# Performance work log

Hardware: AMD Instinct MI355X
Metric: run time of the kernel (lower is better)

Reference implementation:

```python
import jax, jax.numpy as jnp
import numpy as np

ABILITY_SCALE = 3.0

def setup_inputs() -> dict:
    key = jax.random.key(0)
    ks = jax.random.split(key, 20)
    Q, K, M, KD, VD, FD, B, S = 5000, 4, 64, 128, 256, 128, 128, 1024
    g = lambda k, shape: jax.random.normal(k, shape, jnp.float32) * 0.05
    return dict(
        q_data=jax.random.randint(ks[0], (B, S), 0, Q + 1),
        r_data=jax.random.randint(ks[1], (B, S), 0, K),
        q_embed_table=g(ks[2], (Q + 1, KD)),
        key_memory=g(ks[3], (M, KD)),
        init_value_memory=g(ks[4], (M, VD)),
        W_value=g(ks[5], (2 * Q, VD)), b_value=jnp.zeros((VD,), jnp.float32),
        W_erase=g(ks[6], (VD, VD)), b_erase=jnp.zeros((VD,), jnp.float32),
        W_add=g(ks[7], (VD, VD)), b_add=jnp.zeros((VD,), jnp.float32),
        W_summary=g(ks[8], (VD + KD, FD)), b_summary=jnp.zeros((FD,), jnp.float32),
        W_theta=g(ks[9], (FD, 1)), b_theta=jnp.zeros((1,), jnp.float32),
        W_beta=g(ks[10], (KD, K - 1)), b_beta=jnp.zeros((K - 1,), jnp.float32),
        W_disc=g(ks[11], (FD + KD, 1)), b_disc=jnp.zeros((1,), jnp.float32),
        W_c1=g(ks[12], (K + 1, 64)), b_c1=jnp.zeros((64,), jnp.float32),  # irt_dim = 1+1+(K-1)
        W_c2=g(ks[13], (64, 32)), b_c2=jnp.zeros((32,), jnp.float32),
        coral_w=g(ks[14], (32, 1)), coral_b=jnp.zeros((K - 1,), jnp.float32),
    )


def reference(q_data, r_data, q_embed_table, key_memory, init_value_memory,
              W_value, b_value, W_erase, b_erase, W_add, b_add,
              W_summary, b_summary, W_theta, b_theta, W_beta, b_beta,
              W_disc, b_disc, W_c1, b_c1, W_c2, b_c2, coral_w, coral_b):
    B, S = q_data.shape
    Q = W_value.shape[0] // 2
    K = coral_b.shape[0] + 1
    Mv0 = jnp.broadcast_to(init_value_memory[None], (B,) + init_value_memory.shape)

    def step(Mv, qr):
        q_t, r_t = qr  # (B,), (B,)
        qe = q_embed_table[q_t]                                   # (B, KD)
        q1h = jax.nn.one_hot(q_t, Q + 1, dtype=jnp.float32)[:, 1:]  # (B, Q), drop padding id 0
        scale = (r_t.astype(jnp.float32) / (K - 1))[:, None]
        x = jnp.concatenate([q1h, q1h * scale], axis=-1)          # ordered embedding (B, 2Q)
        ve = x @ W_value + b_value                                # (B, VD)
        w = jax.nn.softmax(qe @ key_memory.T, axis=-1)            # (B, M) correlation weight
        read = jnp.einsum('bm,bmv->bv', w, Mv)                    # memory read
        summary = jnp.tanh(jnp.concatenate([read, qe], -1) @ W_summary + b_summary)
        theta = (summary @ W_theta + b_theta)[:, 0] * ABILITY_SCALE
        betas = qe @ W_beta + b_beta                              # (B, K-1)
        alpha = jax.nn.softplus((jnp.concatenate([summary, qe], -1) @ W_disc + b_disc)[:, 0])
        # CORAL head on IRT params
        feat = jnp.concatenate([theta[:, None], alpha[:, None], betas], -1)  # (B, K+1)
        h = jax.nn.relu(feat @ W_c1 + b_c1)
        h = jax.nn.relu(h @ W_c2 + b_c2)
        logits = h @ coral_w + coral_b                            # (B, K-1), shared weight + thresholds
        cum = jnp.cumprod(jax.nn.sigmoid(logits), axis=-1)        # CORN: P(y > k)
        probs = jnp.concatenate([1.0 - cum[:, :1], cum[:, :-1] - cum[:, 1:], cum[:, -1:]], -1)
        # memory write (erase/add)
        erase = jax.nn.sigmoid(ve @ W_erase + b_erase)
        add = jnp.tanh(ve @ W_add + b_add)
        Mv = Mv * (1.0 - w[:, :, None] * erase[:, None, :]) + w[:, :, None] * add[:, None, :]
        return Mv, (theta, betas, alpha, probs, logits)

    _, (thetas, betas, alphas, probs, logits) = jax.lax.scan(
        step, Mv0, (q_data.T, r_data.T))
    tr = lambda a: jnp.swapaxes(a, 0, 1)  # (S, B, ...) -> (B, S, ...)
    return (tr(thetas), tr(betas), tr(alphas), tr(probs), tr(logits))
```

## Files before the change

kernel.cpp:

```cpp
#include <hip/hip_runtime.h>
#include <math.h>

#define BB 128
#define SS 1024
#define MM 64
#define KDIM 128
#define VDIM 256
#define FDIM 128
#define QNUM 5000
#define QD 5001
#define RROWS (4 * QD)

#define QB 16
#define NEA ((QD + QB - 1) / QB)
#define NPRE (NEA + QD + 128)

#define TW 16
#define NWIN (SS / TW)

typedef _Float16 half2_t __attribute__((ext_vector_type(2)));
typedef float f2 __attribute__((ext_vector_type(2)));
typedef _Float16 f16x8 __attribute__((ext_vector_type(8)));
typedef float f32x4 __attribute__((ext_vector_type(4)));

#if defined(__has_builtin)
#if __has_builtin(__builtin_elementwise_fma)
#define HAVE_EFMA 1
#endif
#endif

__device__ __forceinline__ f2 pkfma(f2 a, f2 b, f2 c) {
#ifdef HAVE_EFMA
  return __builtin_elementwise_fma(a, b, c);
#else
  f2 r; r.x = fmaf(a.x, b.x, c.x); r.y = fmaf(a.y, b.y, c.y); return r;
#endif
}

__device__ __forceinline__ float sigmoidf_(float x) { return 1.0f / (1.0f + expf(-x)); }
__device__ __forceinline__ float softplusf_(float x) { return (x > 20.0f) ? x : log1pf(expf(x)); }

__global__ __launch_bounds__(256) void k_pre(
    const float* __restrict__ Wv, const float* __restrict__ bv,
    const float* __restrict__ We, const float* __restrict__ be,
    const float* __restrict__ Wa, const float* __restrict__ ba,
    const float* __restrict__ q_embed, const float* __restrict__ key_mem,
    const float* __restrict__ W_summary, const float* __restrict__ b_summary,
    const float* __restrict__ W_disc,
    const float* __restrict__ W_beta, const float* __restrict__ b_beta,
    float2* __restrict__ EA, float* __restrict__ w_tab,
    float* __restrict__ Sq_tab, float* __restrict__ aq_tab,
    float* __restrict__ beta_tab, _Float16* __restrict__ Wh)
{
  const int tid = threadIdx.x;
  const int blk = blockIdx.x;
  __shared__ __align__(16) float smem[2 * QB * 256];
  __shared__ float s_small[KDIM + MM + FDIM];

  if (blk < NEA) {
    float* su = smem;
    float* sd = smem + QB * 256;
    const int qbase = blk * QB;
#pragma unroll
    for (int j = 0; j < QB; ++j) {
      const int q = qbase + j;
      float u = bv[tid], d = 0.f;
      if (q >= 1 && q < QD) {
        u += Wv[(size_t)(q - 1) * VDIM + tid];
        d = Wv[(size_t)(QNUM + q - 1) * VDIM + tid] * (1.0f / 3.0f);
      }
      su[j * 256 + tid] = u;
      sd[j * 256 + tid] = d;
    }
    __syncthreads();
    f2 aB[QB], aD[QB];
#pragma unroll
    for (int j = 0; j < QB; ++j) { aB[j] = (f2){0.f, 0.f}; aD[j] = (f2){0.f, 0.f}; }
    for (int i = 0; i < 256; i += 4) {
      f2 w0, w1, w2, w3;
      w0.x = We[(i + 0) * VDIM + tid]; w0.y = Wa[(i + 0) * VDIM + tid];
      w1.x = We[(i + 1) * VDIM + tid]; w1.y = Wa[(i + 1) * VDIM + tid];
      w2.x = We[(i + 2) * VDIM + tid]; w2.y = Wa[(i + 2) * VDIM + tid];
      w3.x = We[(i + 3) * VDIM + tid]; w3.y = Wa[(i + 3) * VDIM + tid];
#pragma unroll
      for (int j = 0; j < QB; ++j) {
        const float4 uu = *(const float4*)&su[j * 256 + i];
        const float4 dd = *(const float4*)&sd[j * 256 + i];
        aB[j] = pkfma((f2){uu.x, uu.x}, w0, aB[j]);
        aD[j] = pkfma((f2){dd.x, dd.x}, w0, aD[j]);
        aB[j] = pkfma((f2){uu.y, uu.y}, w1, aB[j]);
        aD[j] = pkfma((f2){dd.y, dd.y}, w1, aD[j]);
        aB[j] = pkfma((f2){uu.z, uu.z}, w2, aB[j]);
        aD[j] = pkfma((f2){dd.z, dd.z}, w2, aD[j]);
        aB[j] = pkfma((f2){uu.w, uu.w}, w3, aB[j]);
        aD[j] = pkfma((f2){dd.w, dd.w}, w3, aD[j]);
      }
    }
    const float bev = be[tid], bav = ba[tid];
#pragma unroll
    for (int j = 0; j < QB; ++j) {
      const int q = qbase + j;
      if (q < QD) {
        const float pe0 = aB[j].x + bev, pa0 = aB[j].y + bav;
        const float de = aD[j].x, da = aD[j].y;
#pragma unroll
        for (int r = 0; r < 4; ++r) {
          float2 p;
          p.x = sigmoidf_(fmaf((float)r, de, pe0));
          p.y = tanhf(fmaf((float)r, da, pa0));
          EA[(size_t)(r * QD + q) * VDIM + tid] = p;
        }
      }
    }
  } else if (blk < NEA + QD) {
    const int q = blk - NEA;
    const int wave = tid >> 6, l = tid & 63;
    float* s_key  = smem;
    float* qe     = s_small;
    float* slog   = s_small + KDIM;
    float* s_half = s_small + KDIM + MM;
    for (int i = tid; i < MM * KDIM; i += 256) s_key[i] = key_mem[i];
    if (tid < KDIM) qe[tid] = q_embed[(size_t)q * KDIM + tid];
    __syncthreads();
    {
      const int m = tid >> 2, j = tid & 3;
      const float* krow = s_key + m * KDIM + j * 32;
      const float* qrow = qe + j * 32;
      float acc = 0.f;
#pragma unroll
      for (int k = 0; k < 32; ++k) {
        const int i = (k + tid) & 31;
        acc = fmaf(qrow[i], krow[i], acc);
      }
      acc += __shfl_xor(acc, 1);
      acc += __shfl_xor(acc, 2);
      if (j == 0) slog[m] = acc;
    }
    __syncthreads();
    if (wave == 0) {
      const float x = slog[l];
      float mx = x;
#pragma unroll
      for (int o = 32; o; o >>= 1) mx = fmaxf(mx, __shfl_xor(mx, o));
      const float e = expf(x - mx);
      float s = e;
#pragma unroll
      for (int o = 32; o; o >>= 1) s += __shfl_xor(s, o);
      w_tab[(size_t)q * MM + l] = e / s;
    } else if (wave == 1) {
      float p = qe[l] * W_disc[KDIM + l] + qe[64 + l] * W_disc[KDIM + 64 + l];
#pragma unroll
      for (int o = 32; o; o >>= 1) p += __shfl_xor(p, o);
      if (l == 0) aq_tab[q] = p;
    } else if (wave == 2) {
      float p0 = qe[l] * W_beta[l * 3 + 0] + qe[64 + l] * W_beta[(64 + l) * 3 + 0];
      float p1 = qe[l] * W_beta[l * 3 + 1] + qe[64 + l] * W_beta[(64 + l) * 3 + 1];
      float p2 = qe[l] * W_beta[l * 3 + 2] + qe[64 + l] * W_beta[(64 + l) * 3 + 2];
#pragma unroll
      for (int o = 32; o; o >>= 1) {
        p0 += __shfl_xor(p0, o); p1 += __shfl_xor(p1, o); p2 += __shfl_xor(p2, o);
      }
      if (l == 0) {
        beta_tab[(size_t)q * 3 + 0] = p0 + b_beta[0];
        beta_tab[(size_t)q * 3 + 1] = p1 + b_beta[1];
        beta_tab[(size_t)q * 3 + 2] = p2 + b_beta[2];
      }
    }
    {
      const int f = tid & 127, h = tid >> 7;
      float acc = 0.f;
#pragma unroll 8
      for (int k = 0; k < 64; ++k)
        acc = fmaf(qe[h * 64 + k], W_summary[(size_t)(VDIM + h * 64 + k) * FDIM + f], acc);
      if (h == 1) s_half[f] = acc;
      __syncthreads();
      if (h == 0) Sq_tab[(size_t)q * FDIM + f] = acc + s_half[f] + b_summary[f];
    }
  } else {
    const int e = (blk - NEA - QD) * 256 + tid;
    const int f = e >> 8, k = e & 255;
    Wh[(size_t)f * 256 + k] = (_Float16)W_summary[(size_t)k * FDIM + f];
  }
}

typedef union { f32x4 v4; f2 h[2]; } Wp;

__global__ __launch_bounds__(512, 4) void k_rec10(
    const int* __restrict__ q_data, const int* __restrict__ r_data,
    const float* __restrict__ init_mv,
    const float2* __restrict__ EA, const float* __restrict__ w_tab,
    _Float16* __restrict__ Rd)
{
  const int tid = threadIdx.x;
  const int lane = tid & 63;
  const int wv = tid >> 6;
  const int b = blockIdx.x >> 2, vc = blockIdx.x & 3;
  const int vv = vc * 64 + lane;
  const int m0 = wv * 8;

  __shared__ int s_off[SS + 32];
  __shared__ int s_q64[SS + 32];
  __shared__ __align__(16) float s_w[2][TW][64];
  __shared__ __align__(16) float s_red[TW][8][64];

  for (int i = tid; i < SS; i += 512) {
    const int q = q_data[b * SS + i];
    const int r = r_data[b * SS + i];
    s_off[i] = (r * QD + q) * (int)(VDIM * sizeof(float2));
    s_q64[i] = q << 6;
  }
  if (tid < 32) { s_off[SS + tid] = 0; s_q64[SS + tid] = 0; }
  __syncthreads();

  {
    const float wa = w_tab[s_q64[wv] + lane];
    const float wb = w_tab[s_q64[wv + 8] + lane];
    s_w[0][wv][lane] = wa;
    s_w[0][wv + 8][lane] = wb;
  }

  f2 mv2[4];
#pragma unroll
  for (int k = 0; k < 4; ++k) {
    mv2[k].x = init_mv[(size_t)(m0 + 2 * k) * VDIM + vv];
    mv2[k].y = init_mv[(size_t)(m0 + 2 * k + 1) * VDIM + vv];
  }

  const char* EAv = (const char*)EA + (size_t)vv * sizeof(float2);

  __syncthreads();

  f2 ear[8];
#pragma unroll
  for (int j = 0; j < 8; ++j)
    ear[j] = *(const f2*)(EAv + (size_t)(unsigned)s_off[j]);

  Wp wl[2], wh[2];

  for (int win = 0; win < NWIN; ++win) {
    const int buf = win & 1;
    const int t0 = win * TW;
    const int tn = ((win + 1) & (NWIN - 1)) * TW + wv;
    const float wstA = w_tab[s_q64[tn] + lane];
    const float wstB = w_tab[s_q64[tn + 8] + lane];
    wl[0].v4 = *(const f32x4*)&s_w[buf][0][m0];
    wh[0].v4 = *(const f32x4*)&s_w[buf][0][m0 + 4];
    wl[1].v4 = *(const f32x4*)&s_w[buf][1][m0];
    wh[1].v4 = *(const f32x4*)&s_w[buf][1][m0 + 4];
#pragma unroll
    for (int tt = 0; tt < TW; ++tt) {
      const int t = t0 + tt;
      const f2 ea = ear[tt & 7];
      const Wp wlo = wl[tt & 1], whi = wh[tt & 1];
      if (tt < TW - 2) {
        wl[tt & 1].v4 = *(const f32x4*)&s_w[buf][tt + 2][m0];
        wh[tt & 1].v4 = *(const f32x4*)&s_w[buf][tt + 2][m0 + 4];
      }
      ear[tt & 7] = *(const f2*)(EAv + (size_t)(unsigned)s_off[t + 8]);
      const f2 e2 = {ea.x, ea.x}, a2 = {ea.y, ea.y};
      f2 rdA = wlo.h[0] * mv2[0];
      rdA = pkfma(wlo.h[1], mv2[1], rdA);
      f2 rdB = whi.h[0] * mv2[2];
      rdB = pkfma(whi.h[1], mv2[3], rdB);
      mv2[0] = pkfma(wlo.h[0], pkfma(-e2, mv2[0], a2), mv2[0]);
      mv2[1] = pkfma(wlo.h[1], pkfma(-e2, mv2[1], a2), mv2[1]);
      mv2[2] = pkfma(whi.h[0], pkfma(-e2, mv2[2], a2), mv2[2]);
      mv2[3] = pkfma(whi.h[1], pkfma(-e2, mv2[3], a2), mv2[3]);
      const f2 rs = rdA + rdB;
      s_red[tt][wv][lane] = rs.x + rs.y;
    }
    __syncthreads();
    {
      s_w[buf ^ 1][wv][lane] = wstA;
      s_w[buf ^ 1][wv + 8][lane] = wstB;
      const int rt = tid >> 5;
      const int vp = (tid & 31) * 2;
      f2 s = *(const f2*)&s_red[rt][0][vp];
#pragma unroll
      for (int k = 1; k < 8; ++k) s += *(const f2*)&s_red[rt][k][vp];
      half2_t hv; hv[0] = (_Float16)s.x; hv[1] = (_Float16)s.y;
      *(half2_t*)&Rd[((size_t)b * SS + t0 + rt) * VDIM + vc * 64 + vp] = hv;
    }
    __syncthreads();
  }
}

__global__ __launch_bounds__(256) void k_head(
    const int* __restrict__ q_data,
    const _Float16* __restrict__ Rd, const _Float16* __restrict__ Wh,
    const float* __restrict__ Sq_tab, const float* __restrict__ aq_tab,
    const float* __restrict__ beta_tab,
    const float* __restrict__ W_theta, const float* __restrict__ b_theta,
    const float* __restrict__ W_disc, const float* __restrict__ b_disc,
    const float* __restrict__ W_c1, const float* __restrict__ b_c1,
    const float* __restrict__ W_c2, const float* __restrict__ b_c2,
    const float* __restrict__ coral_w, const float* __restrict__ coral_b,
    float* __restrict__ out)
{
  const int tid = threadIdx.x;
  const int w = tid >> 6, l = tid & 63;
  const int rowbase = blockIdx.x * 64;
  const int b = rowbase >> 10;
  const int t0 = rowbase & (SS - 1);

  __shared__ __align__(16) _Float16 s_A[64 * 256];
  __shared__ __align__(16) _Float16 s_sum[64 * 128];
  __shared__ __align__(16) float s_h1[4][64];
  __shared__ int   s_q[64];
  __shared__ float s_aq[64];
  __shared__ float s_be[64][3];

  {
    const uint4* src = (const uint4*)(Rd + (size_t)rowbase * VDIM);
    uint4* dst = (uint4*)s_A;
    for (int i = tid; i < (64 * 256 * 2) / 16; i += 256) dst[i] = src[i];
  }
  if (tid < 64) {
    const int q = q_data[b * SS + t0 + tid];
    s_q[tid] = q;
    s_aq[tid] = aq_tab[q];
    s_be[tid][0] = beta_tab[(size_t)q * 3 + 0];
    s_be[tid][1] = beta_tab[(size_t)q * 3 + 1];
    s_be[tid][2] = beta_tab[(size_t)q * 3 + 2];
  }
  __syncthreads();

  {
    const int quad = l >> 4, r16 = l & 15;
    const int mrow = w * 16 + r16;
    f32x4 acc[8];
#pragma unroll
    for (int nt = 0; nt < 8; ++nt) acc[nt] = (f32x4){0.f, 0.f, 0.f, 0.f};
#pragma unroll
    for (int ks = 0; ks < 8; ++ks) {
      const f16x8 afrag = *(const f16x8*)(s_A + mrow * 256 + ks * 32 + quad * 8);
#pragma unroll
      for (int nt = 0; nt < 8; ++nt) {
        const int n = nt * 16 + r16;
        const f16x8 bfrag = *(const f16x8*)(Wh + (size_t)n * 256 + ks * 32 + quad * 8);
        acc[nt] = __builtin_amdgcn_mfma_f32_16x16x32_f16(afrag, bfrag, acc[nt], 0, 0, 0);
      }
    }
#pragma unroll
    for (int nt = 0; nt < 8; ++nt) {
#pragma unroll
      for (int reg = 0; reg < 4; ++reg) {
        const int row = w * 16 + quad * 4 + reg;
        const int col = nt * 16 + r16;
        const float val = acc[nt][reg] + Sq_tab[(size_t)s_q[row] * FDIM + col];
        s_sum[row * 128 + col] = (_Float16)tanhf(val);
      }
    }
  }
  __syncthreads();

  const float tw0 = W_theta[l], tw1 = W_theta[64 + l], tb = b_theta[0];
  const float dw0 = W_disc[l], dw1 = W_disc[64 + l], db = b_disc[0];
  float wc1reg[5];
#pragma unroll
  for (int i = 0; i < 5; ++i) wc1reg[i] = W_c1[i * 64 + l];
  const float bc1 = b_c1[l];
  const int jj = l >> 1, hh2 = l & 1;
  float wc2reg[32];
#pragma unroll
  for (int i = 0; i < 32; ++i) wc2reg[i] = W_c2[(hh2 * 32 + i) * 32 + jj];
  const float bc2 = b_c2[jj];
  const float cw = coral_w[jj];
  const float cb0 = coral_b[0], cb1 = coral_b[1], cb2 = coral_b[2];

  float* out_theta = out;
  float* out_beta  = out + (size_t)BB * SS;
  float* out_alpha = out + (size_t)BB * SS * 4;
  float* out_probs = out + (size_t)BB * SS * 5;
  float* out_logit = out + (size_t)BB * SS * 9;

  for (int rr = 0; rr < 16; ++rr) {
    const int r = w * 16 + rr;
    const float su0 = (float)s_sum[r * 128 + l];
    const float su1 = (float)s_sum[r * 128 + 64 + l];
    float at = su0 * tw0 + su1 * tw1;
    float ad = su0 * dw0 + su1 * dw1;
#pragma unroll
    for (int o = 32; o; o >>= 1) { at += __shfl_xor(at, o); ad += __shfl_xor(ad, o); }
    const float theta = (at + tb) * 3.0f;
    const float alpha = softplusf_(ad + s_aq[r] + db);
    const float be0 = s_be[r][0], be1 = s_be[r][1], be2 = s_be[r][2];
    float h1 = bc1;
    h1 = fmaf(theta, wc1reg[0], h1);
    h1 = fmaf(alpha, wc1reg[1], h1);
    h1 = fmaf(be0, wc1reg[2], h1);
    h1 = fmaf(be1, wc1reg[3], h1);
    h1 = fmaf(be2, wc1reg[4], h1);
    h1 = fmaxf(h1, 0.f);
    s_h1[w][l] = h1;
    float hacc = hh2 ? 0.f : bc2;
    const float4* h4 = (const float4*)s_h1[w];
#pragma unroll
    for (int k = 0; k < 8; ++k) {
      const float4 hv = h4[(hh2 << 3) + k];
      hacc = fmaf(hv.x, wc2reg[4 * k + 0], hacc);
      hacc = fmaf(hv.y, wc2reg[4 * k + 1], hacc);
      hacc = fmaf(hv.z, wc2reg[4 * k + 2], hacc);
      hacc = fmaf(hv.w, wc2reg[4 * k + 3], hacc);
    }
    hacc += __shfl_xor(hacc, 1);
    const float h2 = fmaxf(hacc, 0.f);
    float p = h2 * cw * 0.5f;
#pragma unroll
    for (int o = 32; o; o >>= 1) p += __shfl_xor(p, o);
    if (l == 0) {
      const float z = p;
      const float l0 = z + cb0, l1 = z + cb1, l2 = z + cb2;
      const float s0 = sigmoidf_(l0), s1 = sigmoidf_(l1), s2 = sigmoidf_(l2);
      const float q0 = s0, q1 = s0 * s1, q2 = s0 * s1 * s2;
      const size_t bt = (size_t)rowbase + r;
      out_theta[bt] = theta;
      out_alpha[bt] = alpha;
      out_beta[bt * 3 + 0] = be0;
      out_beta[bt * 3 + 1] = be1;
      out_beta[bt * 3 + 2] = be2;
      out_logit[bt * 3 + 0] = l0;
      out_logit[bt * 3 + 1] = l1;
      out_logit[bt * 3 + 2] = l2;
      out_probs[bt * 4 + 0] = 1.f - q0;
      out_probs[bt * 4 + 1] = q0 - q1;
      out_probs[bt * 4 + 2] = q1 - q2;
      out_probs[bt * 4 + 3] = q2;
    }
  }
}

extern "C" void kernel_launch(void* const* d_in, const int* in_sizes, int n_in,
                              void* d_out, int out_size, void* d_ws, size_t ws_size,
                              hipStream_t stream) {
  const int*   q_data    = (const int*)d_in[0];
  const int*   r_data    = (const int*)d_in[1];
  const float* q_embed   = (const float*)d_in[2];
  const float* key_mem   = (const float*)d_in[3];
  const float* init_mv   = (const float*)d_in[4];
  const float* W_value   = (const float*)d_in[5];
  const float* b_value   = (const float*)d_in[6];
  const float* W_erase   = (const float*)d_in[7];
  const float* b_erase   = (const float*)d_in[8];
  const float* W_add     = (const float*)d_in[9];
  const float* b_add     = (const float*)d_in[10];
  const float* W_summary = (const float*)d_in[11];
  const float* b_summary = (const float*)d_in[12];
  const float* W_theta   = (const float*)d_in[13];
  const float* b_theta   = (const float*)d_in[14];
  const float* W_beta    = (const float*)d_in[15];
  const float* b_beta    = (const float*)d_in[16];
  const float* W_disc    = (const float*)d_in[17];
  const float* b_disc    = (const float*)d_in[18];
  const float* W_c1      = (const float*)d_in[19];
  const float* b_c1      = (const float*)d_in[20];
  const float* W_c2      = (const float*)d_in[21];
  const float* b_c2      = (const float*)d_in[22];
  const float* coral_w   = (const float*)d_in[23];
  const float* coral_b   = (const float*)d_in[24];

  float* ws = (float*)d_ws;
  size_t off = 0;
  float2* EA      = (float2*)(ws + off); off += (size_t)RROWS * VDIM * 2;
  float* w_tab    = ws + off; off += (size_t)QD * MM;
  float* Sq_tab   = ws + off; off += (size_t)QD * FDIM;
  float* aq_tab   = ws + off; off += 5120;
  float* beta_tab = ws + off; off += 15104;
  _Float16* Wh = (_Float16*)(ws + off); off += (VDIM * FDIM) / 2;
  _Float16* Rd = (_Float16*)(ws + off);

  k_pre<<<dim3(NPRE), dim3(256), 0, stream>>>(
      W_value, b_value, W_erase, b_erase, W_add, b_add,
      q_embed, key_mem, W_summary, b_summary, W_disc, W_beta, b_beta,
      EA, w_tab, Sq_tab, aq_tab, beta_tab, Wh);

  k_rec10<<<dim3(BB * 4), dim3(512), 0, stream>>>(
      q_data, r_data, init_mv, EA, w_tab, Rd);

  k_head<<<dim3((BB * SS) / 64), dim3(256), 0, stream>>>(
      q_data, Rd, Wh, Sq_tab, aq_tab, beta_tab,
      W_theta, b_theta, W_disc, b_disc,
      W_c1, b_c1, W_c2, b_c2, coral_w, coral_b, (float*)d_out);
}
```

Measured before the change: 544.6 us.

## Store attention weights in fp16 and vectorize offset prefetch in recurrence

Softmax read weights are stored as fp16 in the precomputed table and in shared memory, so each step loads a single 16-byte vector of eight weights instead of two float4 loads, and the per-window global gather of weights moves half the bytes. The EA gather offsets are now read four at a time as an int4 from shared memory rather than one scalar per step, with the sentinel padding widened to match. This trims LDS traffic and instruction count in the serial inner loop, at the cost of fp16 rounding of the attention weights and extra conversion instructions per step.

```diff
diff --git a/kernel.cpp b/kernel.cpp
--- a/kernel.cpp
+++ b/kernel.cpp
@@ -48,7 +48,7 @@
     const float* __restrict__ W_summary, const float* __restrict__ b_summary,
     const float* __restrict__ W_disc,
     const float* __restrict__ W_beta, const float* __restrict__ b_beta,
-    float2* __restrict__ EA, float* __restrict__ w_tab,
+    float2* __restrict__ EA, _Float16* __restrict__ w_tab,
     float* __restrict__ Sq_tab, float* __restrict__ aq_tab,
     float* __restrict__ beta_tab, _Float16* __restrict__ Wh)
 {
@@ -146,7 +146,7 @@
       float s = e;
 #pragma unroll
       for (int o = 32; o; o >>= 1) s += __shfl_xor(s, o);
-      w_tab[(size_t)q * MM + l] = e / s;
+      w_tab[(size_t)q * MM + l] = (_Float16)(e / s);
     } else if (wave == 1) {
       float p = qe[l] * W_disc[KDIM + l] + qe[64 + l] * W_disc[KDIM + 64 + l];
 #pragma unroll
@@ -183,12 +183,10 @@
   }
 }
 
-typedef union { f32x4 v4; f2 h[2]; } Wp;
-
-__global__ __launch_bounds__(512, 4) void k_rec10(
+__global__ __launch_bounds__(512, 4) void k_rec13(
     const int* __restrict__ q_data, const int* __restrict__ r_data,
     const float* __restrict__ init_mv,
-    const float2* __restrict__ EA, const float* __restrict__ w_tab,
+    const float2* __restrict__ EA, const _Float16* __restrict__ w_tab,
     _Float16* __restrict__ Rd)
 {
   const int tid = threadIdx.x;
@@ -198,9 +196,9 @@
   const int vv = vc * 64 + lane;
   const int m0 = wv * 8;
 
-  __shared__ int s_off[SS + 32];
-  __shared__ int s_q64[SS + 32];
-  __shared__ __align__(16) float s_w[2][TW][64];
+  __shared__ int s_off[SS + 64];
+  __shared__ int s_q64[SS + 64];
+  __shared__ __align__(16) _Float16 s_w16[2][TW][64];
   __shared__ __align__(16) float s_red[TW][8][64];
 
   for (int i = tid; i < SS; i += 512) {
@@ -209,14 +207,14 @@
     s_off[i] = (r * QD + q) * (int)(VDIM * sizeof(float2));
     s_q64[i] = q << 6;
   }
-  if (tid < 32) { s_off[SS + tid] = 0; s_q64[SS + tid] = 0; }
+  if (tid < 64) { s_off[SS + tid] = 0; s_q64[SS + tid] = 0; }
   __syncthreads();
 
   {
-    const float wa = w_tab[s_q64[wv] + lane];
-    const float wb = w_tab[s_q64[wv + 8] + lane];
-    s_w[0][wv][lane] = wa;
-    s_w[0][wv + 8][lane] = wb;
+    const _Float16 wa = w_tab[s_q64[wv] + lane];
+    const _Float16 wb = w_tab[s_q64[wv + 8] + lane];
+    s_w16[0][wv][lane] = wa;
+    s_w16[0][wv + 8][lane] = wb;
   }
 
   f2 mv2[4];
@@ -235,44 +233,48 @@
   for (int j = 0; j < 8; ++j)
     ear[j] = *(const f2*)(EAv + (size_t)(unsigned)s_off[j]);
 
-  Wp wl[2], wh[2];
+  f16x8 wr[2];
 
   for (int win = 0; win < NWIN; ++win) {
     const int buf = win & 1;
     const int t0 = win * TW;
     const int tn = ((win + 1) & (NWIN - 1)) * TW + wv;
-    const float wstA = w_tab[s_q64[tn] + lane];
-    const float wstB = w_tab[s_q64[tn + 8] + lane];
-    wl[0].v4 = *(const f32x4*)&s_w[buf][0][m0];
-    wh[0].v4 = *(const f32x4*)&s_w[buf][0][m0 + 4];
-    wl[1].v4 = *(const f32x4*)&s_w[buf][1][m0];
-    wh[1].v4 = *(const f32x4*)&s_w[buf][1][m0 + 4];
+    const _Float16 wstA = w_tab[s_q64[tn] + lane];
+    const _Float16 wstB = w_tab[s_q64[tn + 8] + lane];
+    wr[0] = *(const f16x8*)&s_w16[buf][0][m0];
+    wr[1] = *(const f16x8*)&s_w16[buf][1][m0];
+    int4 pf;
 #pragma unroll
     for (int tt = 0; tt < TW; ++tt) {
-      const int t = t0 + tt;
+      if ((tt & 3) == 0) pf = *(const int4*)&s_off[t0 + tt + 8];
       const f2 ea = ear[tt & 7];
-      const Wp wlo = wl[tt & 1], whi = wh[tt & 1];
-      if (tt < TW - 2) {
-        wl[tt & 1].v4 = *(const f32x4*)&s_w[buf][tt + 2][m0];
-        wh[tt & 1].v4 = *(const f32x4*)&s_w[buf][tt + 2][m0 + 4];
-      }
-      ear[tt & 7] = *(const f2*)(EAv + (size_t)(unsigned)s_off[t + 8]);
+      const f16x8 wf = wr[tt & 1];
+      if (tt < TW - 2)
+        wr[tt & 1] = *(const f16x8*)&s_w16[buf][tt + 2][m0];
+      {
+        const int po = (tt & 3) == 0 ? pf.x : (tt & 3) == 1 ? pf.y : (tt & 3) == 2 ? pf.z : pf.w;
+        ear[tt & 7] = *(const f2*)(EAv + (size_t)(unsigned)po);
+      }
+      const f2 w0 = {(float)wf[0], (float)wf[1]};
+      const f2 w1 = {(float)wf[2], (float)wf[3]};
+      const f2 w2 = {(float)wf[4], (float)wf[5]};
+      const f2 w3 = {(float)wf[6], (float)wf[7]};
       const f2 e2 = {ea.x, ea.x}, a2 = {ea.y, ea.y};
-      f2 rdA = wlo.h[0] * mv2[0];
-      rdA = pkfma(wlo.h[1], mv2[1], rdA);
-      f2 rdB = whi.h[0] * mv2[2];
-      rdB = pkfma(whi.h[1], mv2[3], rdB);
-      mv2[0] = pkfma(wlo.h[0], pkfma(-e2, mv2[0], a2), mv2[0]);
-      mv2[1] = pkfma(wlo.h[1], pkfma(-e2, mv2[1], a2), mv2[1]);
-      mv2[2] = pkfma(whi.h[0], pkfma(-e2, mv2[2], a2), mv2[2]);
-      mv2[3] = pkfma(whi.h[1], pkfma(-e2, mv2[3], a2), mv2[3]);
+      f2 rdA = w0 * mv2[0];
+      rdA = pkfma(w1, mv2[1], rdA);
+      f2 rdB = w2 * mv2[2];
+      rdB = pkfma(w3, mv2[3], rdB);
+      mv2[0] = pkfma(w0, pkfma(-e2, mv2[0], a2), mv2[0]);
+      mv2[1] = pkfma(w1, pkfma(-e2, mv2[1], a2), mv2[1]);
+      mv2[2] = pkfma(w2, pkfma(-e2, mv2[2], a2), mv2[2]);
+      mv2[3] = pkfma(w3, pkfma(-e2, mv2[3], a2), mv2[3]);
       const f2 rs = rdA + rdB;
       s_red[tt][wv][lane] = rs.x + rs.y;
     }
     __syncthreads();
     {
-      s_w[buf ^ 1][wv][lane] = wstA;
-      s_w[buf ^ 1][wv + 8][lane] = wstB;
+      s_w16[buf ^ 1][wv][lane] = wstA;
+      s_w16[buf ^ 1][wv + 8][lane] = wstB;
       const int rt = tid >> 5;
       const int vp = (tid & 31) * 2;
       f2 s = *(const f2*)&s_red[rt][0][vp];
@@ -462,7 +464,7 @@
   float* ws = (float*)d_ws;
   size_t off = 0;
   float2* EA      = (float2*)(ws + off); off += (size_t)RROWS * VDIM * 2;
-  float* w_tab    = ws + off; off += (size_t)QD * MM;
+  _Float16* w_tab = (_Float16*)(ws + off); off += (size_t)QD * MM;
   float* Sq_tab   = ws + off; off += (size_t)QD * FDIM;
   float* aq_tab   = ws + off; off += 5120;
   float* beta_tab = ws + off; off += 15104;
@@ -474,7 +476,7 @@
       q_embed, key_mem, W_summary, b_summary, W_disc, W_beta, b_beta,
       EA, w_tab, Sq_tab, aq_tab, beta_tab, Wh);
 
-  k_rec10<<<dim3(BB * 4), dim3(512), 0, stream>>>(
+  k_rec13<<<dim3(BB * 4), dim3(512), 0, stream>>>(
       q_data, r_data, init_mv, EA, w_tab, Rd);
 
   k_head<<<dim3((BB * SS) / 64), dim3(256), 0, stream>>>(
```

After: 548.4 us. No clear change (+0.7%).

## Halve recurrence blocks, each thread handling two value columns

Applied to the files above, without the earlier changes.

The recurrence kernel now uses two blocks per batch element instead of four, and each thread updates two value columns (v and v+64) packed into float2. The per-step weight, read-offset and shared-memory reduction costs are spread over twice as much work. Offsets are also fetched four at a time from shared memory. The trade-off is fewer blocks (256 instead of 512), which may leave CUs idle, plus more registers per thread. Launch bounds drop to 2 blocks per CU to match.

```diff
diff --git a/kernel.cpp b/kernel.cpp
--- a/kernel.cpp
+++ b/kernel.cpp
@@ -185,7 +185,7 @@
 
 typedef union { f32x4 v4; f2 h[2]; } Wp;
 
-__global__ __launch_bounds__(512, 4) void k_rec10(
+__global__ __launch_bounds__(512, 2) void k_rec14(
     const int* __restrict__ q_data, const int* __restrict__ r_data,
     const float* __restrict__ init_mv,
     const float2* __restrict__ EA, const float* __restrict__ w_tab,
@@ -194,14 +194,14 @@
   const int tid = threadIdx.x;
   const int lane = tid & 63;
   const int wv = tid >> 6;
-  const int b = blockIdx.x >> 2, vc = blockIdx.x & 3;
-  const int vv = vc * 64 + lane;
+  const int b = blockIdx.x >> 1, vc = blockIdx.x & 1;
+  const int vv = vc * 128 + lane;
   const int m0 = wv * 8;
 
   __shared__ int s_off[SS + 32];
   __shared__ int s_q64[SS + 32];
   __shared__ __align__(16) float s_w[2][TW][64];
-  __shared__ __align__(16) float s_red[TW][8][64];
+  __shared__ __align__(16) f2 s_red[TW][8][64];
 
   for (int i = tid; i < SS; i += 512) {
     const int q = q_data[b * SS + i];
@@ -219,21 +219,23 @@
     s_w[0][wv + 8][lane] = wb;
   }
 
-  f2 mv2[4];
-#pragma unroll
-  for (int k = 0; k < 4; ++k) {
-    mv2[k].x = init_mv[(size_t)(m0 + 2 * k) * VDIM + vv];
-    mv2[k].y = init_mv[(size_t)(m0 + 2 * k + 1) * VDIM + vv];
+  f2 mv[8];
+#pragma unroll
+  for (int k = 0; k < 8; ++k) {
+    mv[k].x = init_mv[(size_t)(m0 + k) * VDIM + vv];
+    mv[k].y = init_mv[(size_t)(m0 + k) * VDIM + vv + 64];
   }
 
   const char* EAv = (const char*)EA + (size_t)vv * sizeof(float2);
 
   __syncthreads();
 
-  f2 ear[8];
-#pragma unroll
-  for (int j = 0; j < 8; ++j)
-    ear[j] = *(const f2*)(EAv + (size_t)(unsigned)s_off[j]);
+  f2 eaL[8], eaH[8];
+#pragma unroll
+  for (int j = 0; j < 8; ++j) {
+    eaL[j] = *(const f2*)(EAv + (size_t)(unsigned)s_off[j]);
+    eaH[j] = *(const f2*)(EAv + (size_t)(unsigned)s_off[j] + 64 * sizeof(float2));
+  }
 
   Wp wl[2], wh[2];
 
@@ -247,39 +249,58 @@
     wh[0].v4 = *(const f32x4*)&s_w[buf][0][m0 + 4];
     wl[1].v4 = *(const f32x4*)&s_w[buf][1][m0];
     wh[1].v4 = *(const f32x4*)&s_w[buf][1][m0 + 4];
+    int4 pf;
 #pragma unroll
     for (int tt = 0; tt < TW; ++tt) {
-      const int t = t0 + tt;
-      const f2 ea = ear[tt & 7];
+      if ((tt & 3) == 0) pf = *(const int4*)&s_off[t0 + tt + 8];
+      const f2 lo = eaL[tt & 7], hi = eaH[tt & 7];
       const Wp wlo = wl[tt & 1], whi = wh[tt & 1];
       if (tt < TW - 2) {
         wl[tt & 1].v4 = *(const f32x4*)&s_w[buf][tt + 2][m0];
         wh[tt & 1].v4 = *(const f32x4*)&s_w[buf][tt + 2][m0 + 4];
       }
-      ear[tt & 7] = *(const f2*)(EAv + (size_t)(unsigned)s_off[t + 8]);
-      const f2 e2 = {ea.x, ea.x}, a2 = {ea.y, ea.y};
-      f2 rdA = wlo.h[0] * mv2[0];
-      rdA = pkfma(wlo.h[1], mv2[1], rdA);
-      f2 rdB = whi.h[0] * mv2[2];
-      rdB = pkfma(whi.h[1], mv2[3], rdB);
-      mv2[0] = pkfma(wlo.h[0], pkfma(-e2, mv2[0], a2), mv2[0]);
-      mv2[1] = pkfma(wlo.h[1], pkfma(-e2, mv2[1], a2), mv2[1]);
-      mv2[2] = pkfma(whi.h[0], pkfma(-e2, mv2[2], a2), mv2[2]);
-      mv2[3] = pkfma(whi.h[1], pkfma(-e2, mv2[3], a2), mv2[3]);
-      const f2 rs = rdA + rdB;
-      s_red[tt][wv][lane] = rs.x + rs.y;
+      {
+        const int po = (tt & 3) == 0 ? pf.x : (tt & 3) == 1 ? pf.y : (tt & 3) == 2 ? pf.z : pf.w;
+        eaL[tt & 7] = *(const f2*)(EAv + (size_t)(unsigned)po);
+        eaH[tt & 7] = *(const f2*)(EAv + (size_t)(unsigned)po + 64 * sizeof(float2));
+      }
+      const f2 e2 = {lo.x, hi.x}, a2 = {lo.y, hi.y};
+      const f2 w0 = {wlo.v4[0], wlo.v4[0]}, w1 = {wlo.v4[1], wlo.v4[1]};
+      const f2 w2 = {wlo.v4[2], wlo.v4[2]}, w3 = {wlo.v4[3], wlo.v4[3]};
+      const f2 w4 = {whi.v4[0], whi.v4[0]}, w5 = {whi.v4[1], whi.v4[1]};
+      const f2 w6 = {whi.v4[2], whi.v4[2]}, w7 = {whi.v4[3], whi.v4[3]};
+      f2 rdA = w0 * mv[0];
+      rdA = pkfma(w1, mv[1], rdA);
+      rdA = pkfma(w2, mv[2], rdA);
+      rdA = pkfma(w3, mv[3], rdA);
+      f2 rdB = w4 * mv[4];
+      rdB = pkfma(w5, mv[5], rdB);
+      rdB = pkfma(w6, mv[6], rdB);
+      rdB = pkfma(w7, mv[7], rdB);
+      mv[0] = pkfma(w0, pkfma(-e2, mv[0], a2), mv[0]);
+      mv[1] = pkfma(w1, pkfma(-e2, mv[1], a2), mv[1]);
+      mv[2] = pkfma(w2, pkfma(-e2, mv[2], a2), mv[2]);
+      mv[3] = pkfma(w3, pkfma(-e2, mv[3], a2), mv[3]);
+      mv[4] = pkfma(w4, pkfma(-e2, mv[4], a2), mv[4]);
+      mv[5] = pkfma(w5, pkfma(-e2, mv[5], a2), mv[5]);
+      mv[6] = pkfma(w6, pkfma(-e2, mv[6], a2), mv[6]);
+      mv[7] = pkfma(w7, pkfma(-e2, mv[7], a2), mv[7]);
+      s_red[tt][wv][lane] = rdA + rdB;
     }
     __syncthreads();
     {
       s_w[buf ^ 1][wv][lane] = wstA;
       s_w[buf ^ 1][wv + 8][lane] = wstB;
       const int rt = tid >> 5;
-      const int vp = (tid & 31) * 2;
-      f2 s = *(const f2*)&s_red[rt][0][vp];
-#pragma unroll
-      for (int k = 1; k < 8; ++k) s += *(const f2*)&s_red[rt][k][vp];
-      half2_t hv; hv[0] = (_Float16)s.x; hv[1] = (_Float16)s.y;
-      *(half2_t*)&Rd[((size_t)b * SS + t0 + rt) * VDIM + vc * 64 + vp] = hv;
+      const int sl0 = (tid & 31) * 2;
+      f32x4 s = *(const f32x4*)&s_red[rt][0][sl0];
+#pragma unroll
+      for (int k = 1; k < 8; ++k) s += *(const f32x4*)&s_red[rt][k][sl0];
+      half2_t hA; hA[0] = (_Float16)s[0]; hA[1] = (_Float16)s[2];
+      half2_t hB; hB[0] = (_Float16)s[1]; hB[1] = (_Float16)s[3];
+      _Float16* rrow = Rd + ((size_t)b * SS + t0 + rt) * VDIM + vc * 128;
+      *(half2_t*)(rrow + sl0) = hA;
+      *(half2_t*)(rrow + 64 + sl0) = hB;
     }
     __syncthreads();
   }
@@ -474,7 +495,7 @@
       q_embed, key_mem, W_summary, b_summary, W_disc, W_beta, b_beta,
       EA, w_tab, Sq_tab, aq_tab, beta_tab, Wh);
 
-  k_rec10<<<dim3(BB * 4), dim3(512), 0, stream>>>(
+  k_rec14<<<dim3(BB * 2), dim3(512), 0, stream>>>(
       q_data, r_data, init_mv, EA, w_tab, Rd);
 
   k_head<<<dim3((BB * SS) / 64), dim3(256), 0, stream>>>(
```

Result: no change. 548.8 us (+0.8%).

## Split recurrence over memory-slot halves with partial read outputs summed in head

Applied to the files above, without the earlier changes.

Adds a new recurrence kernel that gives each block half of the 64 memory slots and 128 value columns, not all 64 slots and 64 columns. Each half writes its partial read vector to a separate fp16 buffer, and the head kernel adds the two buffers while loading them into shared memory. Each lane now covers two value columns, so one gathered erase/add pointer serves twice the work, and the per-step reduction is stored as fp16 in shared memory. The cost is a second global read buffer, extra fp16 rounding before the final sum, and lower occupancy (launch bounds 2 instead of 4). The path is chosen at runtime only when the workspace is large enough, otherwise the old kernel runs.

```diff
diff --git a/kernel.cpp b/kernel.cpp
--- a/kernel.cpp
+++ b/kernel.cpp
@@ -184,6 +184,116 @@
 }
 
 typedef union { f32x4 v4; f2 h[2]; } Wp;
+typedef union { uint2 u; half2_t h[2]; } H4;
+
+__global__ __launch_bounds__(512, 2) void k_rec15(
+    const int* __restrict__ q_data, const int* __restrict__ r_data,
+    const float* __restrict__ init_mv,
+    const float2* __restrict__ EA, const float* __restrict__ w_tab,
+    _Float16* __restrict__ Rd0, _Float16* __restrict__ Rd1)
+{
+  const int tid = threadIdx.x;
+  const int lane = tid & 63;
+  const int wv = tid >> 6;
+  const int idx = blockIdx.x;
+  const int b = idx >> 2, vc = (idx >> 1) & 1, mh = idx & 1;
+  const int vv = vc * 128 + lane;
+  const int mql = mh * 32;
+  const int m0 = mql + wv * 4;
+  _Float16* __restrict__ Rdh = mh ? Rd1 : Rd0;
+
+  __shared__ int s_off[SS + 32];
+  __shared__ int s_q64[SS + 32];
+  __shared__ __align__(16) float s_w[2][TW][32];
+  __shared__ __align__(16) half2_t s_red16[TW][8][64];
+
+  for (int i = tid; i < SS; i += 512) {
+    const int q = q_data[b * SS + i];
+    const int r = r_data[b * SS + i];
+    s_off[i] = (r * QD + q) * (int)(VDIM * sizeof(float2));
+    s_q64[i] = q << 6;
+  }
+  if (tid < 32) { s_off[SS + tid] = 0; s_q64[SS + tid] = 0; }
+  __syncthreads();
+
+  const int srow = tid >> 5, scol = tid & 31;
+  s_w[0][srow][scol] = w_tab[s_q64[srow] + mql + scol];
+
+  f2 mv[4];
+#pragma unroll
+  for (int k = 0; k < 4; ++k) {
+    mv[k].x = init_mv[(size_t)(m0 + k) * VDIM + vv];
+    mv[k].y = init_mv[(size_t)(m0 + k) * VDIM + vv + 64];
+  }
+
+  const char* EAv = (const char*)EA + (size_t)vv * sizeof(float2);
+
+  __syncthreads();
+
+  f2 eaL[8], eaH[8];
+#pragma unroll
+  for (int j = 0; j < 8; ++j) {
+    eaL[j] = *(const f2*)(EAv + (size_t)(unsigned)s_off[j]);
+    eaH[j] = *(const f2*)(EAv + (size_t)(unsigned)s_off[j] + 64 * sizeof(float2));
+  }
+
+  f32x4 wr[2];
+
+  for (int win = 0; win < NWIN; ++win) {
+    const int buf = win & 1;
+    const int t0 = win * TW;
+    const int wn = ((win + 1) & (NWIN - 1)) * TW;
+    const float wst = w_tab[s_q64[wn + srow] + mql + scol];
+    wr[0] = *(const f32x4*)&s_w[buf][0][wv * 4];
+    wr[1] = *(const f32x4*)&s_w[buf][1][wv * 4];
+    int4 pf;
+#pragma unroll
+    for (int tt = 0; tt < TW; ++tt) {
+      if ((tt & 3) == 0) pf = *(const int4*)&s_off[t0 + tt + 8];
+      const f2 lo = eaL[tt & 7], hi = eaH[tt & 7];
+      const f32x4 wq = wr[tt & 1];
+      if (tt < TW - 2)
+        wr[tt & 1] = *(const f32x4*)&s_w[buf][tt + 2][wv * 4];
+      {
+        const int po = (tt & 3) == 0 ? pf.x : (tt & 3) == 1 ? pf.y : (tt & 3) == 2 ? pf.z : pf.w;
+        eaL[tt & 7] = *(const f2*)(EAv + (size_t)(unsigned)po);
+        eaH[tt & 7] = *(const f2*)(EAv + (size_t)(unsigned)po + 64 * sizeof(float2));
+      }
+      const f2 e2 = {lo.x, hi.x}, a2 = {lo.y, hi.y};
+      const f2 w0 = {wq[0], wq[0]}, w1 = {wq[1], wq[1]};
+      const f2 w2 = {wq[2], wq[2]}, w3 = {wq[3], wq[3]};
+      f2 rd = w0 * mv[0];
+      rd = pkfma(w1, mv[1], rd);
+      rd = pkfma(w2, mv[2], rd);
+      rd = pkfma(w3, mv[3], rd);
+      mv[0] = pkfma(w0, pkfma(-e2, mv[0], a2), mv[0]);
+      mv[1] = pkfma(w1, pkfma(-e2, mv[1], a2), mv[1]);
+      mv[2] = pkfma(w2, pkfma(-e2, mv[2], a2), mv[2]);
+      mv[3] = pkfma(w3, pkfma(-e2, mv[3], a2), mv[3]);
+      half2_t h; h[0] = (_Float16)rd.x; h[1] = (_Float16)rd.y;
+      s_red16[tt][wv][lane] = h;
+    }
+    __syncthreads();
+    {
+      s_w[buf ^ 1][srow][scol] = wst;
+      const int rt = tid >> 5;
+      const int sl0 = (tid & 31) * 2;
+      float a0 = 0.f, a1 = 0.f, b0 = 0.f, b1 = 0.f;
+#pragma unroll
+      for (int k = 0; k < 8; ++k) {
+        H4 u; u.u = *(const uint2*)&s_red16[rt][k][sl0];
+        a0 += (float)u.h[0][0]; a1 += (float)u.h[0][1];
+        b0 += (float)u.h[1][0]; b1 += (float)u.h[1][1];
+      }
+      half2_t hA; hA[0] = (_Float16)a0; hA[1] = (_Float16)b0;
+      half2_t hB; hB[0] = (_Float16)a1; hB[1] = (_Float16)b1;
+      _Float16* rrow = Rdh + ((size_t)b * SS + t0 + rt) * VDIM + vc * 128;
+      *(half2_t*)(rrow + sl0) = hA;
+      *(half2_t*)(rrow + 64 + sl0) = hB;
+    }
+    __syncthreads();
+  }
+}
 
 __global__ __launch_bounds__(512, 4) void k_rec10(
     const int* __restrict__ q_data, const int* __restrict__ r_data,
@@ -287,7 +397,8 @@
 
 __global__ __launch_bounds__(256) void k_head(
     const int* __restrict__ q_data,
-    const _Float16* __restrict__ Rd, const _Float16* __restrict__ Wh,
+    const _Float16* __restrict__ Rd0, const _Float16* __restrict__ Rd1, const int two,
+    const _Float16* __restrict__ Wh,
     const float* __restrict__ Sq_tab, const float* __restrict__ aq_tab,
     const float* __restrict__ beta_tab,
     const float* __restrict__ W_theta, const float* __restrict__ b_theta,
@@ -311,9 +422,19 @@
   __shared__ float s_be[64][3];
 
   {
-    const uint4* src = (const uint4*)(Rd + (size_t)rowbase * VDIM);
+    typedef union { uint4 u; f16x8 h; } U8;
+    const uint4* src0 = (const uint4*)(Rd0 + (size_t)rowbase * VDIM);
+    const uint4* src1 = (const uint4*)(Rd1 + (size_t)rowbase * VDIM);
     uint4* dst = (uint4*)s_A;
-    for (int i = tid; i < (64 * 256 * 2) / 16; i += 256) dst[i] = src[i];
+    if (two) {
+      for (int i = tid; i < (64 * 256 * 2) / 16; i += 256) {
+        U8 a, c; a.u = src0[i]; c.u = src1[i];
+        a.h = a.h + c.h;
+        dst[i] = a.u;
+      }
+    } else {
+      for (int i = tid; i < (64 * 256 * 2) / 16; i += 256) dst[i] = src0[i];
+    }
   }
   if (tid < 64) {
     const int q = q_data[b * SS + t0 + tid];
@@ -467,18 +588,27 @@
   float* aq_tab   = ws + off; off += 5120;
   float* beta_tab = ws + off; off += 15104;
   _Float16* Wh = (_Float16*)(ws + off); off += (VDIM * FDIM) / 2;
-  _Float16* Rd = (_Float16*)(ws + off);
+  _Float16* Rd0 = (_Float16*)(ws + off);
+  const size_t rd_half = (size_t)BB * SS * VDIM;
+  _Float16* Rd1 = Rd0 + rd_half;
+  const size_t need_bytes = off * sizeof(float) + 2 * rd_half * sizeof(_Float16);
+  const int two = (ws_size >= need_bytes) ? 1 : 0;
 
   k_pre<<<dim3(NPRE), dim3(256), 0, stream>>>(
       W_value, b_value, W_erase, b_erase, W_add, b_add,
       q_embed, key_mem, W_summary, b_summary, W_disc, W_beta, b_beta,
       EA, w_tab, Sq_tab, aq_tab, beta_tab, Wh);
 
-  k_rec10<<<dim3(BB * 4), dim3(512), 0, stream>>>(
-      q_data, r_data, init_mv, EA, w_tab, Rd);
+  if (two) {
+    k_rec15<<<dim3(BB * 4), dim3(512), 0, stream>>>(
+        q_data, r_data, init_mv, EA, w_tab, Rd0, Rd1);
+  } else {
+    k_rec10<<<dim3(BB * 4), dim3(512), 0, stream>>>(
+        q_data, r_data, init_mv, EA, w_tab, Rd0);
+  }
 
   k_head<<<dim3((BB * SS) / 64), dim3(256), 0, stream>>>(
-      q_data, Rd, Wh, Sq_tab, aq_tab, beta_tab,
+      q_data, Rd0, Rd1, two, Wh, Sq_tab, aq_tab, beta_tab,
       W_theta, b_theta, W_disc, b_disc,
       W_c1, b_c1, W_c2, b_c2, coral_w, coral_b, (float*)d_out);
 }
```

Result: slower. 658.8 us (+21.0%).
